# Kernel tuning notes

Measured on AMD Instinct MI355X. Metric: run time of the kernel, lower is better.

Reference implementation:

```python
import jax, jax.numpy as jnp
import numpy as np

N_NODES = 100000
N_EDGES = 800000
D_IN = 128
D_HID = 128
N_CLASSES = 64


def _glorot(key, shape):
    fan_in, fan_out = shape[0], shape[1]
    lim = jnp.sqrt(6.0 / (fan_in + fan_out)).astype(jnp.float32)
    return jax.random.uniform(key, shape, jnp.float32, -lim, lim)


def setup_inputs() -> dict:
    key = jax.random.key(0)
    ks = jax.random.split(key, 20)
    inp = {
        "x": jax.random.normal(ks[0], (N_NODES, D_IN), jnp.float32),
        "edge_src": jax.random.randint(ks[1], (N_EDGES,), 0, N_NODES, jnp.int32),
        "edge_dst": jax.random.randint(ks[2], (N_EDGES,), 0, N_NODES, jnp.int32),
    }
    dims = [(D_IN, D_HID), (D_HID, D_HID), (D_HID, N_CLASSES)]
    k = 3
    for i, (di, do) in enumerate(dims):
        inp[f"Wp{i}"] = _glorot(ks[k], (di, di)); k += 1   # fc_pool: d_in -> d_in
        inp[f"bp{i}"] = jnp.zeros((di,), jnp.float32)
        inp[f"Ws{i}"] = _glorot(ks[k], (di, do)); k += 1   # fc_self (no bias)
        inp[f"Wn{i}"] = _glorot(ks[k], (di, do)); k += 1   # fc_neigh
        inp[f"bn{i}"] = jnp.zeros((do,), jnp.float32)
    return inp


def _sage_pool_layer(x, src, dst, Wp, bp, Ws, Wn, bn):
    # pool aggregator: max over in-edges of relu(fc_pool(h_src))
    m = jax.nn.relu(x @ Wp + bp)                 # [N, d_in]
    msg = m[src]                                 # [E, d_in] gather
    agg = jax.ops.segment_max(msg, dst, num_segments=N_NODES)  # scatter-max
    agg = jnp.where(jnp.isfinite(agg), agg, 0.0)  # zero-in-degree nodes -> 0
    return x @ Ws + agg @ Wn + bn


def reference(x, edge_src, edge_dst,
              Wp0, bp0, Ws0, Wn0, bn0,
              Wp1, bp1, Ws1, Wn1, bn1,
              Wp2, bp2, Ws2, Wn2, bn2):
    layers = [
        (Wp0, bp0, Ws0, Wn0, bn0),
        (Wp1, bp1, Ws1, Wn1, bn1),
        (Wp2, bp2, Ws2, Wn2, bn2),
    ]
    h = x
    for (Wp, bp, Ws, Wn, bn) in layers:
        # SAGEConv internal activation=relu followed by wrapper F.relu (idempotent)
        h = jax.nn.relu(_sage_pool_layer(h, edge_src, edge_dst, Wp, bp, Ws, Wn, bn))
    return jax.nn.log_softmax(h, axis=-1)
```

## Files before the change

kernel.cpp:

```cpp
#include <hip/hip_runtime.h>
#include <cstddef>
#include <cstdint>

#define NNODES 100000
#define NEDGES 800000
#define CAP 32
#define NXCD 8

typedef unsigned short u16;
typedef __attribute__((ext_vector_type(8))) short short8;
typedef __attribute__((ext_vector_type(8))) _Float16 half8;
typedef __attribute__((ext_vector_type(4))) float f32x4;
typedef __attribute__((ext_vector_type(4))) int int4v;

__device__ __forceinline__ u16 f32_to_bf16(float f) {
    union { float f; uint32_t u; } v; v.f = f;
    uint32_t r = v.u + 0x7FFF + ((v.u >> 16) & 1);
    return (u16)(r >> 16);
}
__device__ __forceinline__ u16 f32_to_f16(float f) {
    union { _Float16 h; u16 u; } v; v.h = (_Float16)f;
    return v.u;
}
__device__ __forceinline__ uint32_t pkmax(uint32_t a, uint32_t b) {
    uint32_t lo = max(a & 0xFFFFu, b & 0xFFFFu);
    uint32_t hi = max(a >> 16, b >> 16);
    return lo | (hi << 16);
}

__global__ __launch_bounds__(256) void zero_kernel(float4* __restrict__ p, int n4) {
    int i = blockIdx.x * blockDim.x + threadIdx.x;
    const int stride = gridDim.x * blockDim.x;
    for (; i < n4; i += stride) p[i] = make_float4(0.f, 0.f, 0.f, 0.f);
}

__global__ __launch_bounds__(256) void fill_bucket_kernel(
    const int* __restrict__ src, const int4v* __restrict__ dst4,
    int* __restrict__ deg, int* __restrict__ col2, int E4)
{
    const int xcd  = blockIdx.x & (NXCD - 1);
    const int grp  = blockIdx.x >> 3;
    const int ngrp = gridDim.x >> 3;
    const int lo = xcd * (NNODES / NXCD);
    const int hi = lo + (NNODES / NXCD);

    for (int i = grp * 256 + threadIdx.x; i < E4; i += ngrp * 256) {
        const int4v d4 = __builtin_nontemporal_load(&dst4[i]);
        const int e = i * 4;
#pragma unroll
        for (int j = 0; j < 4; ++j) {
            const int d = d4[j];
            if (d >= lo && d < hi) {
                const int r = atomicAdd(&deg[d], 1);
                if (r < CAP)
                    col2[d * CAP + r] = __builtin_nontemporal_load(&src[e + j]);
            }
        }
    }
}

__global__ __launch_bounds__(256) void bf16_cast_kernel(
    const float4* __restrict__ in, uint2* __restrict__ out, int n4)
{
    int i = blockIdx.x * 256 + threadIdx.x;
    const int stride = gridDim.x * 256;
    for (; i < n4; i += stride) {
        float4 v = in[i];
        out[i] = make_uint2(
            (uint32_t)f32_to_bf16(v.x) | ((uint32_t)f32_to_bf16(v.y) << 16),
            (uint32_t)f32_to_bf16(v.z) | ((uint32_t)f32_to_bf16(v.w) << 16));
    }
}

struct WPtrs { const float* w[9]; };

__global__ __launch_bounds__(256) void split_weights_kernel(WPtrs p, u16* __restrict__ wbase)
{
    const int idx = blockIdx.x * 256 + threadIdx.x;
    const int w = blockIdx.y;
    const int DO_ = (w >= 7) ? 64 : 128;
    if (idx >= 128 * DO_) return;
    const float v = p.w[w][idx];
    const int k = idx / DO_;
    const int c = idx - k * DO_;
    const bool use_f16 = (w == 2 || w == 5 || w == 8);
    wbase[w * 32768 + c * 128 + k] = use_f16 ? f32_to_f16(v) : f32_to_bf16(v);
}

__global__ __launch_bounds__(256) void copy_w_kernel(
    const uint32_t* __restrict__ w7, const uint32_t* __restrict__ w8,
    uint32_t* __restrict__ dstw)
{
    int i = blockIdx.x * 256 + threadIdx.x;
    if (i < 4096) dstw[i] = w7[i];
    else if (i < 8192) dstw[i] = w8[i - 4096];
}

template<int DO, bool DUAL, int OUT_MODE>
__global__ __launch_bounds__(512, 4) void mfma_gemm_kernel(
    const u16* __restrict__ A,
    const u16* __restrict__ Cq,
    const u16* __restrict__ WaT, const u16* __restrict__ WbT,
    const float* __restrict__ bias,
    float* __restrict__ outF, u16* __restrict__ outU,
    int N)
{
    constexpr int CT = DO / 16;
    constexpr int WS = 136;
    __shared__ u16 sW[(DUAL ? 2 : 1) * DO * WS];

    const int tid = threadIdx.x;

    for (int i = tid; i < DO * 16; i += 512) {
        const int r = i >> 4;
        const int c = (i & 15) << 3;
        *(short8*)&sW[r * WS + c] = *(const short8*)&WaT[r * 128 + c];
        if constexpr (DUAL)
            *(short8*)&sW[DO * WS + r * WS + c] = *(const short8*)&WbT[r * 128 + c];
    }

    const int lane = tid & 63;
    const int wid  = tid >> 6;
    const int l15  = lane & 15;
    const int lk   = (lane >> 4) << 3;
    const int row0 = blockIdx.x * 256 + wid * 32;

    int aoff0, aoff1;
    {
        int r0 = row0 + l15;      if (r0 > N - 1) r0 = N - 1;
        int r1 = row0 + 16 + l15; if (r1 > N - 1) r1 = N - 1;
        aoff0 = r0 * 128 + lk;
        aoff1 = r1 * 128 + lk;
    }

    f32x4 acc[2][CT];
#pragma unroll
    for (int m = 0; m < 2; ++m)
#pragma unroll
        for (int c = 0; c < CT; ++c) acc[m][c] = (f32x4){0.f, 0.f, 0.f, 0.f};

    __syncthreads();

#pragma unroll
    for (int k = 0; k < 4; ++k) {
        const int ko = 32 * k;
        short8 ah0 = *(const short8*)(A + aoff0 + ko);
        short8 ah1 = *(const short8*)(A + aoff1 + ko);
        half8 ch0, ch1;
        if constexpr (DUAL) {
            ch0 = *(const half8*)(Cq + aoff0 + ko);
            ch1 = *(const half8*)(Cq + aoff1 + ko);
        }
#pragma unroll
        for (int ct = 0; ct < CT; ++ct) {
            const int wb = (ct * 16 + l15) * WS + lk + ko;
            short8 wh = *(const short8*)&sW[wb];
            acc[0][ct] = __builtin_amdgcn_mfma_f32_16x16x32_bf16(ah0, wh, acc[0][ct], 0, 0, 0);
            acc[1][ct] = __builtin_amdgcn_mfma_f32_16x16x32_bf16(ah1, wh, acc[1][ct], 0, 0, 0);
            if constexpr (DUAL) {
                half8 vh = *(const half8*)&sW[DO * WS + wb];
                acc[0][ct] = __builtin_amdgcn_mfma_f32_16x16x32_f16(ch0, vh, acc[0][ct], 0, 0, 0);
                acc[1][ct] = __builtin_amdgcn_mfma_f32_16x16x32_f16(ch1, vh, acc[1][ct], 0, 0, 0);
            }
        }
    }

    float bv[CT];
#pragma unroll
    for (int ct = 0; ct < CT; ++ct) bv[ct] = bias[ct * 16 + l15];

    const int jrow = (lane >> 4) << 2;
#pragma unroll
    for (int m = 0; m < 2; ++m) {
#pragma unroll
        for (int j = 0; j < 4; ++j) {
            const int r = row0 + m * 16 + jrow + j;
            if constexpr (OUT_MODE == 3) {
                float v[CT];
                float mx = 0.f;
#pragma unroll
                for (int ct = 0; ct < CT; ++ct) {
                    v[ct] = fmaxf(acc[m][ct][j] + bv[ct], 0.f);
                    mx = fmaxf(mx, v[ct]);
                }
#pragma unroll
                for (int off = 1; off < 16; off <<= 1) mx = fmaxf(mx, __shfl_xor(mx, off));
                float s = 0.f;
#pragma unroll
                for (int ct = 0; ct < CT; ++ct) s += __expf(v[ct] - mx);
#pragma unroll
                for (int off = 1; off < 16; off <<= 1) s += __shfl_xor(s, off);
                const float lse = mx + __logf(s);
                if (r < N) {
#pragma unroll
                    for (int ct = 0; ct < CT; ++ct)
                        outF[(size_t)r * DO + ct * 16 + l15] = v[ct] - lse;
                }
            } else if (r < N) {
#pragma unroll
                for (int ct = 0; ct < CT; ++ct) {
                    float v = fmaxf(acc[m][ct][j] + bv[ct], 0.f);
                    const size_t o = (size_t)r * DO + ct * 16 + l15;
                    if constexpr (OUT_MODE == 0) {
                        outF[o] = v;
                    } else if constexpr (OUT_MODE == 1) {
                        outU[o] = f32_to_bf16(v);
                    } else if constexpr (OUT_MODE == 2) {
                        outU[o] = f32_to_f16(v);
                    }
                }
            }
        }
    }
}

__global__ __launch_bounds__(256) void aggregate_kernel(
    const uint4* __restrict__ m4,
    const int* __restrict__ deg,
    const int* __restrict__ col2,
    uint4* __restrict__ agg4, int N)
{
    const int tid  = threadIdx.x;
    const int l16  = tid & 15;
    const int node = (blockIdx.x * 256 + tid) >> 4;
    if (node >= N) return;
    int cnt = deg[node];
    if (cnt > CAP) cnt = CAP;
    const int base = node * CAP;

    uint32_t a0 = 0, a1 = 0, a2 = 0, a3 = 0;
    int e = 0;
    for (; e + 4 <= cnt; e += 4) {
        const int s0 = col2[base + e],     s1 = col2[base + e + 1];
        const int s2 = col2[base + e + 2], s3 = col2[base + e + 3];
        const uint4 v0 = m4[(size_t)s0 * 16 + l16];
        const uint4 v1 = m4[(size_t)s1 * 16 + l16];
        const uint4 v2 = m4[(size_t)s2 * 16 + l16];
        const uint4 v3 = m4[(size_t)s3 * 16 + l16];
        a0 = pkmax(a0, v0.x); a1 = pkmax(a1, v0.y); a2 = pkmax(a2, v0.z); a3 = pkmax(a3, v0.w);
        a0 = pkmax(a0, v1.x); a1 = pkmax(a1, v1.y); a2 = pkmax(a2, v1.z); a3 = pkmax(a3, v1.w);
        a0 = pkmax(a0, v2.x); a1 = pkmax(a1, v2.y); a2 = pkmax(a2, v2.z); a3 = pkmax(a3, v2.w);
        a0 = pkmax(a0, v3.x); a1 = pkmax(a1, v3.y); a2 = pkmax(a2, v3.z); a3 = pkmax(a3, v3.w);
    }
    for (; e < cnt; ++e) {
        const uint4 v0 = m4[(size_t)col2[base + e] * 16 + l16];
        a0 = pkmax(a0, v0.x); a1 = pkmax(a1, v0.y); a2 = pkmax(a2, v0.z); a3 = pkmax(a3, v0.w);
    }
    agg4[(size_t)node * 16 + l16] = make_uint4(a0, a1, a2, a3);
}

extern "C" void kernel_launch(void* const* d_in, const int* in_sizes, int n_in,
                              void* d_out, int out_size, void* d_ws, size_t ws_size,
                              hipStream_t stream)
{
    const int N = NNODES, E = NEDGES;
    const float* x  = (const float*)d_in[0];
    const int* esrc = (const int*)d_in[1];
    const int* edst = (const int*)d_in[2];
    const float* bp[3] = {(const float*)d_in[4], (const float*)d_in[9],  (const float*)d_in[14]};
    const float* bn[3] = {(const float*)d_in[7], (const float*)d_in[12], (const float*)d_in[17]};

    char* ws = (char*)d_ws;
    const size_t P = (size_t)N * 128 * 2;
    u16* p0 = (u16*)(ws);
    u16* p2 = (u16*)(ws + 2 * P);
    u16* p4 = (u16*)(ws + 4 * P);
    u16* p5 = (u16*)(ws + 5 * P);

    char* ob = (char*)d_out;
    int* deg    = (int*)ob;
    int* col2   = (int*)(ob + 409600);
    u16* wbase  = (u16*)(ob + 409600 + (size_t)N * CAP * 4);
    auto WT = [&](int i) { return wbase + i * 32768; };

    const int gblocks = (N + 255) / 256;
    const int ablocks = (N * 16 + 255) / 256;
    dim3 blk(256), gblk(512);

    zero_kernel<<<128, blk, 0, stream>>>((float4*)deg, N / 4);
    fill_bucket_kernel<<<2048, blk, 0, stream>>>(esrc, (const int4v*)edst, deg, col2, E / 4);

    WPtrs wp;
    wp.w[0] = (const float*)d_in[3];  wp.w[1] = (const float*)d_in[5];  wp.w[2] = (const float*)d_in[6];
    wp.w[3] = (const float*)d_in[8];  wp.w[4] = (const float*)d_in[10]; wp.w[5] = (const float*)d_in[11];
    wp.w[6] = (const float*)d_in[13]; wp.w[7] = (const float*)d_in[15]; wp.w[8] = (const float*)d_in[16];
    split_weights_kernel<<<dim3(64, 9), blk, 0, stream>>>(wp, wbase);
    bf16_cast_kernel<<<2048, blk, 0, stream>>>((const float4*)x, (uint2*)p0, N * 128 / 4);

    mfma_gemm_kernel<128, false, 2><<<gblocks, gblk, 0, stream>>>(
        p0, nullptr, WT(0), nullptr, bp[0], nullptr, p4, N);
    aggregate_kernel<<<ablocks, blk, 0, stream>>>((const uint4*)p4, deg, col2, (uint4*)p5, N);
    mfma_gemm_kernel<128, true, 1><<<gblocks, gblk, 0, stream>>>(
        p0, p5, WT(1), WT(2), bn[0], nullptr, p2, N);

    mfma_gemm_kernel<128, false, 2><<<gblocks, gblk, 0, stream>>>(
        p2, nullptr, WT(3), nullptr, bp[1], nullptr, p4, N);
    aggregate_kernel<<<ablocks, blk, 0, stream>>>((const uint4*)p4, deg, col2, (uint4*)p5, N);
    mfma_gemm_kernel<128, true, 1><<<gblocks, gblk, 0, stream>>>(
        p2, p5, WT(4), WT(5), bn[1], nullptr, p0, N);

    mfma_gemm_kernel<128, false, 2><<<gblocks, gblk, 0, stream>>>(
        p0, nullptr, WT(6), nullptr, bp[2], nullptr, p4, N);
    aggregate_kernel<<<ablocks, blk, 0, stream>>>((const uint4*)p4, deg, col2, (uint4*)p5, N);
    copy_w_kernel<<<32, blk, 0, stream>>>((const uint32_t*)WT(7), (const uint32_t*)WT(8), (uint32_t*)p4);
    mfma_gemm_kernel<64, true, 3><<<gblocks, gblk, 0, stream>>>(
        p0, p5, p4, p4 + 8192, bn[2], (float*)d_out, nullptr, N);
}
```

Measured before the change: 264.6 us.

## Fuse prologue kernels, shrink GEMM tile, read second weight from global

Merges edge bucketing, input bf16 cast and weight transposition into a single prologue launch. Moves scratch buffers from the output into the workspace, which removes the final weight copy kernel. The GEMM now processes 128 rows per block with a single M tile per wave, and loads the neighbour weight operand directly from global memory instead of LDS. This cuts launch overhead and LDS usage but may add global load latency in the inner loop.

```diff
diff --git a/kernel.cpp b/kernel.cpp
--- a/kernel.cpp
+++ b/kernel.cpp
@@ -34,182 +34,54 @@
     for (; i < n4; i += stride) p[i] = make_float4(0.f, 0.f, 0.f, 0.f);
 }
 
-__global__ __launch_bounds__(256) void fill_bucket_kernel(
+struct WPtrs { const float* w[9]; };
+
+__global__ __launch_bounds__(256) void prologue_kernel(
     const int* __restrict__ src, const int4v* __restrict__ dst4,
-    int* __restrict__ deg, int* __restrict__ col2, int E4)
-{
-    const int xcd  = blockIdx.x & (NXCD - 1);
-    const int grp  = blockIdx.x >> 3;
-    const int ngrp = gridDim.x >> 3;
-    const int lo = xcd * (NNODES / NXCD);
-    const int hi = lo + (NNODES / NXCD);
-
-    for (int i = grp * 256 + threadIdx.x; i < E4; i += ngrp * 256) {
-        const int4v d4 = __builtin_nontemporal_load(&dst4[i]);
-        const int e = i * 4;
-#pragma unroll
-        for (int j = 0; j < 4; ++j) {
-            const int d = d4[j];
-            if (d >= lo && d < hi) {
-                const int r = atomicAdd(&deg[d], 1);
-                if (r < CAP)
-                    col2[d * CAP + r] = __builtin_nontemporal_load(&src[e + j]);
-            }
-        }
-    }
-}
-
-__global__ __launch_bounds__(256) void bf16_cast_kernel(
-    const float4* __restrict__ in, uint2* __restrict__ out, int n4)
-{
-    int i = blockIdx.x * 256 + threadIdx.x;
-    const int stride = gridDim.x * 256;
-    for (; i < n4; i += stride) {
-        float4 v = in[i];
-        out[i] = make_uint2(
-            (uint32_t)f32_to_bf16(v.x) | ((uint32_t)f32_to_bf16(v.y) << 16),
-            (uint32_t)f32_to_bf16(v.z) | ((uint32_t)f32_to_bf16(v.w) << 16));
-    }
-}
-
-struct WPtrs { const float* w[9]; };
-
-__global__ __launch_bounds__(256) void split_weights_kernel(WPtrs p, u16* __restrict__ wbase)
-{
-    const int idx = blockIdx.x * 256 + threadIdx.x;
-    const int w = blockIdx.y;
-    const int DO_ = (w >= 7) ? 64 : 128;
-    if (idx >= 128 * DO_) return;
-    const float v = p.w[w][idx];
-    const int k = idx / DO_;
-    const int c = idx - k * DO_;
-    const bool use_f16 = (w == 2 || w == 5 || w == 8);
-    wbase[w * 32768 + c * 128 + k] = use_f16 ? f32_to_f16(v) : f32_to_bf16(v);
-}
-
-__global__ __launch_bounds__(256) void copy_w_kernel(
-    const uint32_t* __restrict__ w7, const uint32_t* __restrict__ w8,
-    uint32_t* __restrict__ dstw)
-{
-    int i = blockIdx.x * 256 + threadIdx.x;
-    if (i < 4096) dstw[i] = w7[i];
-    else if (i < 8192) dstw[i] = w8[i - 4096];
-}
-
-template<int DO, bool DUAL, int OUT_MODE>
-__global__ __launch_bounds__(512, 4) void mfma_gemm_kernel(
-    const u16* __restrict__ A,
-    const u16* __restrict__ Cq,
-    const u16* __restrict__ WaT, const u16* __restrict__ WbT,
-    const float* __restrict__ bias,
-    float* __restrict__ outF, u16* __restrict__ outU,
-    int N)
-{
-    constexpr int CT = DO / 16;
-    constexpr int WS = 136;
-    __shared__ u16 sW[(DUAL ? 2 : 1) * DO * WS];
-
+    int* __restrict__ deg, int* __restrict__ col2, int E4,
+    const float4* __restrict__ x4, uint2* __restrict__ xb, int n4,
+    WPtrs p, u16* __restrict__ wbase)
+{
+    const int b = blockIdx.x;
     const int tid = threadIdx.x;
 
-    for (int i = tid; i < DO * 16; i += 512) {
-        const int r = i >> 4;
-        const int c = (i & 15) << 3;
-        *(short8*)&sW[r * WS + c] = *(const short8*)&WaT[r * 128 + c];
-        if constexpr (DUAL)
-            *(short8*)&sW[DO * WS + r * WS + c] = *(const short8*)&WbT[r * 128 + c];
-    }
-
-    const int lane = tid & 63;
-    const int wid  = tid >> 6;
-    const int l15  = lane & 15;
-    const int lk   = (lane >> 4) << 3;
-    const int row0 = blockIdx.x * 256 + wid * 32;
-
-    int aoff0, aoff1;
-    {
-        int r0 = row0 + l15;      if (r0 > N - 1) r0 = N - 1;
-        int r1 = row0 + 16 + l15; if (r1 > N - 1) r1 = N - 1;
-        aoff0 = r0 * 128 + lk;
-        aoff1 = r1 * 128 + lk;
-    }
-
-    f32x4 acc[2][CT];
-#pragma unroll
-    for (int m = 0; m < 2; ++m)
-#pragma unroll
-        for (int c = 0; c < CT; ++c) acc[m][c] = (f32x4){0.f, 0.f, 0.f, 0.f};
-
-    __syncthreads();
-
-#pragma unroll
-    for (int k = 0; k < 4; ++k) {
-        const int ko = 32 * k;
-        short8 ah0 = *(const short8*)(A + aoff0 + ko);
-        short8 ah1 = *(const short8*)(A + aoff1 + ko);
-        half8 ch0, ch1;
-        if constexpr (DUAL) {
-            ch0 = *(const half8*)(Cq + aoff0 + ko);
-            ch1 = *(const half8*)(Cq + aoff1 + ko);
-        }
-#pragma unroll
-        for (int ct = 0; ct < CT; ++ct) {
-            const int wb = (ct * 16 + l15) * WS + lk + ko;
-            short8 wh = *(const short8*)&sW[wb];
-            acc[0][ct] = __builtin_amdgcn_mfma_f32_16x16x32_bf16(ah0, wh, acc[0][ct], 0, 0, 0);
-            acc[1][ct] = __builtin_amdgcn_mfma_f32_16x16x32_bf16(ah1, wh, acc[1][ct], 0, 0, 0);
-            if constexpr (DUAL) {
-                half8 vh = *(const half8*)&sW[DO * WS + wb];
-                acc[0][ct] = __builtin_amdgcn_mfma_f32_16x16x32_f16(ch0, vh, acc[0][ct], 0, 0, 0);
-                acc[1][ct] = __builtin_amdgcn_mfma_f32_16x16x32_f16(ch1, vh, acc[1][ct], 0, 0, 0);
-            }
-        }
-    }
-
-    float bv[CT];
-#pragma unroll
-    for (int ct = 0; ct < CT; ++ct) bv[ct] = bias[ct * 16 + l15];
-
-    const int jrow = (lane >> 4) << 2;
-#pragma unroll
-    for (int m = 0; m < 2; ++m) {
-#pragma unroll
-        for (int j = 0; j < 4; ++j) {
-            const int r = row0 + m * 16 + jrow + j;
-            if constexpr (OUT_MODE == 3) {
-                float v[CT];
-                float mx = 0.f;
-#pragma unroll
-                for (int ct = 0; ct < CT; ++ct) {
-                    v[ct] = fmaxf(acc[m][ct][j] + bv[ct], 0.f);
-                    mx = fmaxf(mx, v[ct]);
+    if (b < 2048) {
+        const int xcd  = b & (NXCD - 1);
+        const int grp  = b >> 3;
+        const int ngrp = 2048 >> 3;
+        const int lo = xcd * (NNODES / NXCD);
+        const int hi = lo + (NNODES / NXCD);
+        for (int i = grp * 256 + tid; i < E4; i += ngrp * 256) {
+            const int4v d4 = __builtin_nontemporal_load(&dst4[i]);
+            const int e = i * 4;
+#pragma unroll
+            for (int j = 0; j < 4; ++j) {
+                const int d = d4[j];
+                if (d >= lo && d < hi) {
+                    const int r = atomicAdd(&deg[d], 1);
+                    if (r < CAP)
+                        col2[d * CAP + r] = __builtin_nontemporal_load(&src[e + j]);
                 }
-#pragma unroll
-                for (int off = 1; off < 16; off <<= 1) mx = fmaxf(mx, __shfl_xor(mx, off));
-                float s = 0.f;
-#pragma unroll
-                for (int ct = 0; ct < CT; ++ct) s += __expf(v[ct] - mx);
-#pragma unroll
-                for (int off = 1; off < 16; off <<= 1) s += __shfl_xor(s, off);
-                const float lse = mx + __logf(s);
-                if (r < N) {
-#pragma unroll
-                    for (int ct = 0; ct < CT; ++ct)
-                        outF[(size_t)r * DO + ct * 16 + l15] = v[ct] - lse;
-                }
-            } else if (r < N) {
-#pragma unroll
-                for (int ct = 0; ct < CT; ++ct) {
-                    float v = fmaxf(acc[m][ct][j] + bv[ct], 0.f);
-                    const size_t o = (size_t)r * DO + ct * 16 + l15;
-                    if constexpr (OUT_MODE == 0) {
-                        outF[o] = v;
-                    } else if constexpr (OUT_MODE == 1) {
-                        outU[o] = f32_to_bf16(v);
-                    } else if constexpr (OUT_MODE == 2) {
-                        outU[o] = f32_to_f16(v);
-                    }
-                }
-            }
+            }
+        }
+    } else if (b < 4096) {
+        for (int i = (b - 2048) * 256 + tid; i < n4; i += 2048 * 256) {
+            float4 v = x4[i];
+            xb[i] = make_uint2(
+                (uint32_t)f32_to_bf16(v.x) | ((uint32_t)f32_to_bf16(v.y) << 16),
+                (uint32_t)f32_to_bf16(v.z) | ((uint32_t)f32_to_bf16(v.w) << 16));
+        }
+    } else {
+        const int wb = b - 4096;
+        const int w = wb >> 6;
+        const int DO_ = (w >= 7) ? 64 : 128;
+        const int idx = ((wb & 63) << 8) | tid;
+        if (idx < 128 * DO_) {
+            const float v = p.w[w][idx];
+            const int k = idx / DO_;
+            const int c = idx - k * DO_;
+            const bool use_f16 = (w == 2 || w == 5 || w == 8);
+            wbase[w * 32768 + c * 128 + k] = use_f16 ? f32_to_f16(v) : f32_to_bf16(v);
         }
     }
 }
@@ -249,6 +121,103 @@
     agg4[(size_t)node * 16 + l16] = make_uint4(a0, a1, a2, a3);
 }
 
+template<int DO, bool DUAL, int OUT_MODE>
+__global__ __launch_bounds__(512, 4) void mfma_gemm_kernel(
+    const u16* __restrict__ A,
+    const u16* __restrict__ Cq,
+    const u16* __restrict__ WaT, const u16* __restrict__ WbT,
+    const float* __restrict__ bias,
+    float* __restrict__ outF, u16* __restrict__ outU, int N)
+{
+    constexpr int CT = DO / 16;
+    constexpr int WS = 136;
+    __shared__ u16 sW[DO * WS];
+
+    const int tid = threadIdx.x;
+    for (int i = tid; i < DO * 16; i += 512) {
+        const int r = i >> 4;
+        const int c = (i & 15) << 3;
+        *(short8*)&sW[r * WS + c] = *(const short8*)&WaT[r * 128 + c];
+    }
+
+    const int lane = tid & 63;
+    const int wid  = tid >> 6;
+    const int l15  = lane & 15;
+    const int sec  = lane >> 4;
+    const int lk   = sec << 3;
+    const int row0 = blockIdx.x * 128 + wid * 16;
+
+    int aoff;
+    {
+        int r = row0 + l15; if (r > N - 1) r = N - 1;
+        aoff = r * 128 + lk;
+    }
+
+    f32x4 acc[CT];
+#pragma unroll
+    for (int c = 0; c < CT; ++c) acc[c] = (f32x4){0.f, 0.f, 0.f, 0.f};
+
+    __syncthreads();
+
+#pragma unroll
+    for (int k = 0; k < 4; ++k) {
+        const int ko = 32 * k;
+        short8 ah = *(const short8*)(A + aoff + ko);
+        half8 ch;
+        if constexpr (DUAL) ch = *(const half8*)(Cq + aoff + ko);
+#pragma unroll
+        for (int ct = 0; ct < CT; ++ct) {
+            const int wrow = ct * 16 + l15;
+            short8 wh = *(const short8*)&sW[wrow * WS + lk + ko];
+            acc[ct] = __builtin_amdgcn_mfma_f32_16x16x32_bf16(ah, wh, acc[ct], 0, 0, 0);
+            if constexpr (DUAL) {
+                half8 vh = *(const half8*)(WbT + wrow * 128 + lk + ko);
+                acc[ct] = __builtin_amdgcn_mfma_f32_16x16x32_f16(ch, vh, acc[ct], 0, 0, 0);
+            }
+        }
+    }
+
+    float bv[CT];
+#pragma unroll
+    for (int ct = 0; ct < CT; ++ct) bv[ct] = bias[ct * 16 + l15];
+
+    const int jrow = sec << 2;
+#pragma unroll
+    for (int j = 0; j < 4; ++j) {
+        const int r = row0 + jrow + j;
+        if constexpr (OUT_MODE == 3) {
+            float v[CT];
+            float mx = 0.f;
+#pragma unroll
+            for (int ct = 0; ct < CT; ++ct) {
+                v[ct] = fmaxf(acc[ct][j] + bv[ct], 0.f);
+                mx = fmaxf(mx, v[ct]);
+            }
+#pragma unroll
+            for (int off = 1; off < 16; off <<= 1) mx = fmaxf(mx, __shfl_xor(mx, off));
+            float s = 0.f;
+#pragma unroll
+            for (int ct = 0; ct < CT; ++ct) s += __expf(v[ct] - mx);
+#pragma unroll
+            for (int off = 1; off < 16; off <<= 1) s += __shfl_xor(s, off);
+            const float lse = mx + __logf(s);
+            if (r < N) {
+#pragma unroll
+                for (int ct = 0; ct < CT; ++ct)
+                    outF[(size_t)r * DO + ct * 16 + l15] = v[ct] - lse;
+            }
+        } else if (r < N) {
+#pragma unroll
+            for (int ct = 0; ct < CT; ++ct) {
+                float v = fmaxf(acc[ct][j] + bv[ct], 0.f);
+                const size_t o = (size_t)r * DO + ct * 16 + l15;
+                if constexpr (OUT_MODE == 1) outU[o] = f32_to_bf16(v);
+                else                          outU[o] = f32_to_f16(v);
+            }
+        }
+    }
+}
+
 extern "C" void kernel_launch(void* const* d_in, const int* in_sizes, int n_in,
                               void* d_out, int out_size, void* d_ws, size_t ws_size,
                               hipStream_t stream)
@@ -263,46 +232,44 @@
     char* ws = (char*)d_ws;
     const size_t P = (size_t)N * 128 * 2;
     u16* p0 = (u16*)(ws);
+    char* p1 = ws + P;
     u16* p2 = (u16*)(ws + 2 * P);
+    u16* wbase = (u16*)(ws + 3 * P);
     u16* p4 = (u16*)(ws + 4 * P);
     u16* p5 = (u16*)(ws + 5 * P);
 
-    char* ob = (char*)d_out;
-    int* deg    = (int*)ob;
-    int* col2   = (int*)(ob + 409600);
-    u16* wbase  = (u16*)(ob + 409600 + (size_t)N * CAP * 4);
+    int* deg  = (int*)p1;
+    int* col2 = (int*)(p1 + 409600);
     auto WT = [&](int i) { return wbase + i * 32768; };
 
-    const int gblocks = (N + 255) / 256;
+    const int gg = (N + 127) / 128;
     const int ablocks = (N * 16 + 255) / 256;
     dim3 blk(256), gblk(512);
 
-    zero_kernel<<<128, blk, 0, stream>>>((float4*)deg, N / 4);
-    fill_bucket_kernel<<<2048, blk, 0, stream>>>(esrc, (const int4v*)edst, deg, col2, E / 4);
-
+    zero_kernel<<<128, blk, 0, stream>>>((float4*)p1, 409600 / 16);
     WPtrs wp;
     wp.w[0] = (const float*)d_in[3];  wp.w[1] = (const float*)d_in[5];  wp.w[2] = (const float*)d_in[6];
     wp.w[3] = (const float*)d_in[8];  wp.w[4] = (const float*)d_in[10]; wp.w[5] = (const float*)d_in[11];
     wp.w[6] = (const float*)d_in[13]; wp.w[7] = (const float*)d_in[15]; wp.w[8] = (const float*)d_in[16];
-    split_weights_kernel<<<dim3(64, 9), blk, 0, stream>>>(wp, wbase);
-    bf16_cast_kernel<<<2048, blk, 0, stream>>>((const float4*)x, (uint2*)p0, N * 128 / 4);
-
-    mfma_gemm_kernel<128, false, 2><<<gblocks, gblk, 0, stream>>>(
+    prologue_kernel<<<4672, blk, 0, stream>>>(
+        esrc, (const int4v*)edst, deg, col2, E / 4,
+        (const float4*)x, (uint2*)p0, N * 128 / 4, wp, wbase);
+
+    mfma_gemm_kernel<128, false, 2><<<gg, gblk, 0, stream>>>(
         p0, nullptr, WT(0), nullptr, bp[0], nullptr, p4, N);
     aggregate_kernel<<<ablocks, blk, 0, stream>>>((const uint4*)p4, deg, col2, (uint4*)p5, N);
-    mfma_gemm_kernel<128, true, 1><<<gblocks, gblk, 0, stream>>>(
+    mfma_gemm_kernel<128, true, 1><<<gg, gblk, 0, stream>>>(
         p0, p5, WT(1), WT(2), bn[0], nullptr, p2, N);
 
-    mfma_gemm_kernel<128, false, 2><<<gblocks, gblk, 0, stream>>>(
+    mfma_gemm_kernel<128, false, 2><<<gg, gblk, 0, stream>>>(
         p2, nullptr, WT(3), nullptr, bp[1], nullptr, p4, N);
     aggregate_kernel<<<ablocks, blk, 0, stream>>>((const uint4*)p4, deg, col2, (uint4*)p5, N);
-    mfma_gemm_kernel<128, true, 1><<<gblocks, gblk, 0, stream>>>(
+    mfma_gemm_kernel<128, true, 1><<<gg, gblk, 0, stream>>>(
         p2, p5, WT(4), WT(5), bn[1], nullptr, p0, N);
 
-    mfma_gemm_kernel<128, false, 2><<<gblocks, gblk, 0, stream>>>(
+    mfma_gemm_kernel<128, false, 2><<<gg, gblk, 0, stream>>>(
         p0, nullptr, WT(6), nullptr, bp[2], nullptr, p4, N);
     aggregate_kernel<<<ablocks, blk, 0, stream>>>((const uint4*)p4, deg, col2, (uint4*)p5, N);
-    copy_w_kernel<<<32, blk, 0, stream>>>((const uint32_t*)WT(7), (const uint32_t*)WT(8), (uint32_t*)p4);
-    mfma_gemm_kernel<64, true, 3><<<gblocks, gblk, 0, stream>>>(
-        p0, p5, p4, p4 + 8192, bn[2], (float*)d_out, nullptr, N);
-}
+    mfma_gemm_kernel<64, true, 3><<<gg, gblk, 0, stream>>>(
+        p0, p5, WT(7), WT(8), bn[2], (float*)d_out, nullptr, N);
+}
```

After: 323.8 us. 22.4% more time.
